# Optimization experiments

Hardware: AMD Instinct MI355X
Metric: run time of the kernel (lower is better)

Reference implementation:

```python
import jax, jax.numpy as jnp
from jax import lax
import numpy as np

FEAT_STRIDE = 16
N_PRE_NMS = 6000
N_POST_NMS = 300
NMS_THRESH = 0.7
MIN_SIZE = 16.0
HH, WW = 100, 152  # feature map size
IN_C, MID_C, N_ANCHOR = 512, 512, 9


def _anchor_base(base=16.0, ratios=(0.5, 1.0, 2.0), scales=(8, 16, 32)):
    py, px = base / 2.0, base / 2.0
    ab = np.zeros((len(ratios) * len(scales), 4), np.float32)
    for i, r in enumerate(ratios):
        for j, s in enumerate(scales):
            h = base * s * np.sqrt(r)
            w = base * s * np.sqrt(1.0 / r)
            ab[i * len(scales) + j] = [py - h / 2, px - w / 2, py + h / 2, px + w / 2]
    return ab


def _shifted_anchors(hh, ww, stride=FEAT_STRIDE):
    ab = _anchor_base()
    sy = np.arange(hh, dtype=np.float32) * stride
    sx = np.arange(ww, dtype=np.float32) * stride
    sx, sy = np.meshgrid(sx, sy)
    shift = np.stack((sy.ravel(), sx.ravel(), sy.ravel(), sx.ravel()), axis=1)
    # [K,A,4] -> [K*A,4]: location-major, anchor-minor (matches loc reshape order)
    return (shift[:, None, :] + ab[None, :, :]).reshape(-1, 4).astype(np.float32)


def _conv2d(x, w, b, pad):
    y = lax.conv_general_dilated(x, w, (1, 1), [(pad, pad), (pad, pad)],
                                 dimension_numbers=("NCHW", "OIHW", "NCHW"))
    return y + b[None, :, None, None]


def _loc2bbox(anchor, loc):
    h = anchor[:, 2] - anchor[:, 0]
    w = anchor[:, 3] - anchor[:, 1]
    cy = anchor[:, 0] + 0.5 * h
    cx = anchor[:, 1] + 0.5 * w
    dy, dx, dh, dw = loc[:, 0], loc[:, 1], loc[:, 2], loc[:, 3]
    cy2 = dy * h + cy
    cx2 = dx * w + cx
    h2 = jnp.exp(dh) * h
    w2 = jnp.exp(dw) * w
    return jnp.stack([cy2 - 0.5 * h2, cx2 - 0.5 * w2, cy2 + 0.5 * h2, cx2 + 0.5 * w2], axis=1)


def _nms_keep(boxes, thresh):
    # boxes sorted by score desc; sequential greedy NMS via fori_loop over a
    # precomputed [N,N] IoU matrix.
    N = boxes.shape[0]
    y1, x1, y2, x2 = boxes[:, 0], boxes[:, 1], boxes[:, 2], boxes[:, 3]
    area = (y2 - y1) * (x2 - x1)
    ih = jnp.clip(jnp.minimum(y2[:, None], y2[None, :]) - jnp.maximum(y1[:, None], y1[None, :]), 0.0)
    iw = jnp.clip(jnp.minimum(x2[:, None], x2[None, :]) - jnp.maximum(x1[:, None], x1[None, :]), 0.0)
    inter = ih * iw
    iou = inter / (area[:, None] + area[None, :] - inter + 1e-9)
    idx = jnp.arange(N)

    def body(i, keep):
        sup = keep[i] & (iou[i] > thresh) & (idx > i)
        return keep & ~sup

    return lax.fori_loop(0, N, body, jnp.ones((N,), bool))


def setup_inputs() -> dict:
    key = jax.random.key(0)
    ks = jax.random.split(key, 4)
    return {
        "x": jax.random.normal(ks[0], (1, IN_C, HH, WW), jnp.float32),
        "conv1_w": 0.01 * jax.random.normal(ks[1], (MID_C, IN_C, 3, 3), jnp.float32),
        "conv1_b": jnp.zeros((MID_C,), jnp.float32),
        "score_w": 0.01 * jax.random.normal(ks[2], (N_ANCHOR * 2, MID_C, 1, 1), jnp.float32),
        "score_b": jnp.zeros((N_ANCHOR * 2,), jnp.float32),
        "loc_w": 0.01 * jax.random.normal(ks[3], (N_ANCHOR * 4, MID_C, 1, 1), jnp.float32),
        "loc_b": jnp.zeros((N_ANCHOR * 4,), jnp.float32),
        "img_h": 1600,
        "img_w": 2432,
    }


def reference(x, conv1_w, conv1_b, score_w, score_b, loc_w, loc_b, img_h, img_w):
    n, _, hh, ww = x.shape
    anchors = jnp.asarray(_shifted_anchors(hh, ww))  # [hh*ww*A, 4]

    h = jax.nn.relu(_conv2d(x, conv1_w, conv1_b, 1))
    rpn_loc = _conv2d(h, loc_w, loc_b, 0).transpose(0, 2, 3, 1).reshape(n, -1, 4)
    scores_hw = _conv2d(h, score_w, score_b, 0).transpose(0, 2, 3, 1)  # [n,hh,ww,2A]
    fg = jax.nn.softmax(scores_hw.reshape(n, hh, ww, N_ANCHOR, 2), axis=-1)[..., 1].reshape(n, -1)
    rpn_score = scores_hw.reshape(n, -1, 2)

    # ProposalCreator (single image)
    roi = _loc2bbox(anchors, rpn_loc[0])
    roi = jnp.stack([
        jnp.clip(roi[:, 0], 0.0, img_h), jnp.clip(roi[:, 1], 0.0, img_w),
        jnp.clip(roi[:, 2], 0.0, img_h), jnp.clip(roi[:, 3], 0.0, img_w)], axis=1)
    valid = ((roi[:, 2] - roi[:, 0]) >= MIN_SIZE) & ((roi[:, 3] - roi[:, 1]) >= MIN_SIZE)
    sc = jnp.where(valid, fg[0], -jnp.inf)

    top_sc, order = lax.top_k(sc, N_PRE_NMS)
    roi_s = roi[order]  # sorted by score desc
    keep = _nms_keep(lax.stop_gradient(roi_s), NMS_THRESH) & (top_sc > -jnp.inf)
    sel_sc, sel = lax.top_k(jnp.where(keep, top_sc, -jnp.inf), N_POST_NMS)
    rois = jnp.where((sel_sc > -jnp.inf)[:, None], roi_s[sel], 0.0)  # [N_POST_NMS,4], zero-padded
    return rpn_loc, rpn_score, rois
```

## Files before the change

kernel.cpp:

```cpp
#include <hip/hip_runtime.h>
#include <math.h>
#include <stdint.h>

#define CHH 100
#define CWW 152
#define NPIX 15200
#define NANCH 136800
#define NPRE 6000
#define NPOST 300
#define CANDCAP 8192
#define MROW 96

#define PSTRIDE 154
#define PPVALID 16016
#define PPS 16128
#define XGUARD 256
#define XROWS_TOTAL (PPS + 2*XGUARD)

#define LPAD 32

#define WTH_OFF  0ull
#define WTL_OFF  4718592ull
#define WX_OFF   9437184ull
#define XH_OFF   9547776ull
#define XL_OFF   26587136ull
#define H_OFF    43626496ull
#define ROI_OFF  76656640ull
#define SC_OFF   78845440ull
#define CTL_OFF  79392640ull
#define CAND_OFF 79396736ull
#define SBOX_OFF 79462272ull

typedef _Float16 f16x8 __attribute__((ext_vector_type(8)));
typedef float    f32x4 __attribute__((ext_vector_type(4)));

struct Ctl {
  unsigned hist[256];
  unsigned prefix;
  unsigned countGreater;
  unsigned candCount;
  unsigned done;
};

struct AnchorArg { float v[36]; };

__device__ __forceinline__ unsigned mono_key(float f) {
  unsigned u = __float_as_uint(f);
  return u ^ ((u & 0x80000000u) ? 0xFFFFFFFFu : 0x80000000u);
}

__device__ __forceinline__ void async_copy16(void* lds, const void* g) {
  __builtin_amdgcn_global_load_lds(
      (const __attribute__((address_space(1))) unsigned int*)g,
      (__attribute__((address_space(3))) unsigned int*)lds,
      16, 0, 0);
}

__global__ __launch_bounds__(256) void prep_w_kernel(const float* __restrict__ w1,
                                                     _Float16* __restrict__ wtapH,
                                                     _Float16* __restrict__ wtapL,
                                                     const float* __restrict__ score_w,
                                                     const float* __restrict__ loc_w,
                                                     float* __restrict__ wx,
                                                     Ctl* __restrict__ ctl) {
  __shared__ float wl[4608];
  const int oc = blockIdx.x, tid = threadIdx.x;
  if (oc == 0) {
    ctl->hist[tid] = 0u;
    if (tid == 0) { ctl->prefix = 0u; ctl->countGreater = 0u; ctl->candCount = 0u; ctl->done = 0u; }
  }
  if (tid < 54) wx[oc * 54 + tid] = (tid < 18) ? score_w[tid * 512 + oc] : loc_w[(tid - 18) * 512 + oc];
  for (int li = tid; li < 4608; li += 256) wl[li] = w1[(size_t)oc * 4608 + li];
  __syncthreads();
  for (int t = 0; t < 9; ++t) {
    size_t ob = ((size_t)t * 512 + oc) * 512;
    for (int ic = tid; ic < 512; ic += 256) {
      float v = wl[ic * 9 + t];
      _Float16 hi = (_Float16)v;
      wtapH[ob + ic] = hi;
      wtapL[ob + ic] = (_Float16)(v - (float)hi);
    }
  }
}

__global__ __launch_bounds__(256) void prep_x_kernel(const float* __restrict__ x,
                                                     _Float16* __restrict__ xh,
                                                     _Float16* __restrict__ xl) {
  __shared__ float tile[64][65];
  const int tid = threadIdx.x;
  const int r0 = blockIdx.x * 64;
  for (int ic0 = 0; ic0 < 512; ic0 += 64) {
    #pragma unroll
    for (int it = 0; it < 16; ++it) {
      int li = it * 256 + tid;
      int i = li >> 6, j = li & 63;
      int pp = r0 + j - XGUARD;
      float v = 0.f;
      if (pp >= 0 && pp < PPVALID) {
        int rowp = pp / PSTRIDE, colp = pp - rowp * PSTRIDE;
        if (rowp >= 1 && rowp <= 100 && colp >= 1 && colp <= 152) {
          int p = (rowp - 1) * CWW + (colp - 1);
          v = x[(size_t)(ic0 + i) * NPIX + p];
        }
      }
      tile[i][j] = v;
    }
    __syncthreads();
    int j = tid >> 2, cq = tid & 3;
    size_t ob = (size_t)(r0 + j) * 512 + ic0 + cq * 16;
    f16x8 vh0, vh1, vl0, vl1;
    #pragma unroll
    for (int c = 0; c < 8; ++c) {
      float v = tile[cq * 16 + c][j];
      _Float16 hi = (_Float16)v;
      vh0[c] = hi; vl0[c] = (_Float16)(v - (float)hi);
    }
    #pragma unroll
    for (int c = 0; c < 8; ++c) {
      float v = tile[cq * 16 + 8 + c][j];
      _Float16 hi = (_Float16)v;
      vh1[c] = hi; vl1[c] = (_Float16)(v - (float)hi);
    }
    *(f16x8*)&xh[ob]     = vh0;
    *(f16x8*)&xh[ob + 8] = vh1;
    *(f16x8*)&xl[ob]     = vl0;
    *(f16x8*)&xl[ob + 8] = vl1;
    __syncthreads();
  }
}

__global__ __launch_bounds__(256) void conv1_mfma_kernel(const _Float16* __restrict__ xh,
                                                         const _Float16* __restrict__ xl,
                                                         const _Float16* __restrict__ wtapH,
                                                         const _Float16* __restrict__ wtapL,
                                                         const float* __restrict__ bias,
                                                         float* __restrict__ h) {
  __shared__ _Float16 Ah[2][128][LPAD], Al[2][128][LPAD], Bh[2][128][LPAD], Bl[2][128][LPAD];
  __shared__ float bsm[128];
  const int tid = threadIdx.x;
  const int bid = blockIdx.x;
  const int oc0 = (bid & 3) * 128;
  const int pp0 = (((bid >> 3) << 1) + ((bid >> 2) & 1)) * 128;
  if (tid < 128) bsm[tid] = bias[oc0 + tid];

  const int lane = tid & 63;
  const int n16 = lane & 15, quad = lane >> 4;
  const int wid = tid >> 6;
  const int wm = wid >> 1, wn = wid & 1;
  const int srow = tid >> 2, sq = tid & 3;
  const int wrow = wid << 4;
  const int sqs  = sq ^ ((srow >> 1) & 3);
  const int cswz = (n16 >> 1) & 3;
  const int rdc  = (quad ^ cswz) * 8;

  const size_t thBase = (size_t)srow * 512 + (size_t)sqs * 8;

  f32x4 acc[4][4];
  #pragma unroll
  for (int mi = 0; mi < 4; ++mi)
    #pragma unroll
    for (int ni = 0; ni < 4; ++ni) acc[mi][ni] = (f32x4){0.f, 0.f, 0.f, 0.f};

  auto stageF = [&](int b, int t, int icb, int dsh) {
    const size_t wOff = ((size_t)t * 512 + oc0) * 512 + (size_t)icb;
    const size_t xOff = (size_t)(pp0 + dsh) * 512 + (size_t)icb;
    #pragma unroll
    for (int hf = 0; hf < 2; ++hf) {
      const int lrow = hf * 64 + wrow;
      const size_t tho = thBase + (size_t)(hf * 64) * 512;
      async_copy16(&Ah[b][lrow][0], wtapH + wOff + tho);
      async_copy16(&Al[b][lrow][0], wtapL + wOff + tho);
      async_copy16(&Bh[b][lrow][0], xh + xOff + tho);
      async_copy16(&Bl[b][lrow][0], xl + xOff + tho);
    }
  };

  stageF(0, 0, 0, -PSTRIDE - 1);
  int tS = 1, icbS = 0, dshS = -PSTRIDE;

  asm volatile("s_waitcnt vmcnt(0)" ::: "memory");
  __builtin_amdgcn_sched_barrier(0);
  __builtin_amdgcn_s_barrier();
  __builtin_amdgcn_sched_barrier(0);

  for (int ks = 0; ks < 144; ++ks) {
    const int cur = ks & 1;
    if (ks + 1 < 144) {
      stageF(cur ^ 1, tS, icbS, dshS);
      if (++tS == 9) { tS = 0; icbS += 32; dshS = -PSTRIDE - 1; }
      else dshS += (tS == 3 || tS == 6) ? (PSTRIDE - 2) : 1;
    }

    __builtin_amdgcn_s_setprio(1);
    f16x8 af[4], ag[4], bf[4], bg[4];
    #pragma unroll
    for (int mi = 0; mi < 4; ++mi) {
      af[mi] = *(const f16x8*)&Ah[cur][wm * 64 + mi * 16 + n16][rdc];
      ag[mi] = *(const f16x8*)&Al[cur][wm * 64 + mi * 16 + n16][rdc];
    }
    #pragma unroll
    for (int ni = 0; ni < 4; ++ni) {
      bf[ni] = *(const f16x8*)&Bh[cur][wn * 64 + ni * 16 + n16][rdc];
      bg[ni] = *(const f16x8*)&Bl[cur][wn * 64 + ni * 16 + n16][rdc];
    }
    #pragma unroll
    for (int mi = 0; mi < 4; ++mi)
      #pragma unroll
      for (int ni = 0; ni < 4; ++ni) {
        acc[mi][ni] = __builtin_amdgcn_mfma_f32_16x16x32_f16(af[mi], bf[ni], acc[mi][ni], 0, 0, 0);
        acc[mi][ni] = __builtin_amdgcn_mfma_f32_16x16x32_f16(af[mi], bg[ni], acc[mi][ni], 0, 0, 0);
        acc[mi][ni] = __builtin_amdgcn_mfma_f32_16x16x32_f16(ag[mi], bf[ni], acc[mi][ni], 0, 0, 0);
      }
    __builtin_amdgcn_s_setprio(0);

    asm volatile("s_waitcnt lgkmcnt(0) vmcnt(0)" ::: "memory");
    __builtin_amdgcn_sched_barrier(0);
    __builtin_amdgcn_s_barrier();
    __builtin_amdgcn_sched_barrier(0);
  }

  #pragma unroll
  for (int mi = 0; mi < 4; ++mi) {
    int ocb = wm * 64 + mi * 16 + quad * 4;
    #pragma unroll
    for (int ni = 0; ni < 4; ++ni) {
      int pp = pp0 + wn * 64 + ni * 16 + n16;
      #pragma unroll
      for (int r = 0; r < 4; ++r) {
        float v = acc[mi][ni][r] + bsm[ocb + r];
        h[(size_t)(oc0 + ocb + r) * PPS + pp] = fmaxf(v, 0.f);
      }
    }
  }
}

__global__ __launch_bounds__(256) void heads_kernel(const float* __restrict__ h,
                                                    const float* __restrict__ wx,
                                                    const float* __restrict__ score_b,
                                                    const float* __restrict__ loc_b,
                                                    float* __restrict__ rpn_loc,
                                                    float* __restrict__ rpn_score,
                                                    float* __restrict__ roi,
                                                    float* __restrict__ sc,
                                                    AnchorArg ab,
                                                    const int* __restrict__ ihp,
                                                    const int* __restrict__ iwp) {
  __shared__ float hs[64][64];
  __shared__ float red[54][64];
  const int tid = threadIdx.x;
  const int p0 = blockIdx.x * 64;
  const int pxl = tid & 63, icq = tid >> 6;
  int pcol = p0 + pxl;
  bool pok = pcol < NPIX;
  int ppl = 0;
  if (pok) ppl = (pcol / CWW + 1) * PSTRIDE + (pcol % CWW) + 1;

  float acc[54];
  #pragma unroll
  for (int o = 0; o < 54; ++o) acc[o] = 0.f;

  for (int c = 0; c < 8; ++c) {
    int ic0 = c * 64;
    #pragma unroll
    for (int r = 0; r < 16; ++r) {
      int i = r * 4 + icq;
      hs[i][pxl] = pok ? h[(size_t)(ic0 + i) * PPS + ppl] : 0.f;
    }
    __syncthreads();
    #pragma unroll
    for (int k = 0; k < 16; ++k) {
      int icl = icq + k * 4;
      float v = hs[icl][pxl];
      const float* wrow = &wx[(ic0 + icl) * 54];
      #pragma unroll
      for (int o = 0; o < 54; ++o) acc[o] += wrow[o] * v;
    }
    __syncthreads();
  }
  for (int w = 0; w < 4; ++w) {
    if (icq == w) {
      if (w == 0) {
        #pragma unroll
        for (int o = 0; o < 54; ++o) red[o][pxl] = acc[o];
      } else {
        #pragma unroll
        for (int o = 0; o < 54; ++o) red[o][pxl] += acc[o];
      }
    }
    __syncthreads();
  }

  const float fH = (float)(*ihp);
  const float fW = (float)(*iwp);
  for (int it = tid; it < 576; it += 256) {
    #pragma clang fp contract(off)
    int pl = it / 9, a = it - pl * 9;
    int p = p0 + pl;
    if (p >= NPIX) continue;
    float s0 = red[a * 2][pl]     + score_b[a * 2];
    float s1 = red[a * 2 + 1][pl] + score_b[a * 2 + 1];
    float dy = red[18 + a * 4][pl]     + loc_b[a * 4];
    float dx = red[18 + a * 4 + 1][pl] + loc_b[a * 4 + 1];
    float dh = red[18 + a * 4 + 2][pl] + loc_b[a * 4 + 2];
    float dw = red[18 + a * 4 + 3][pl] + loc_b[a * 4 + 3];
    int row = p * 9 + a;
    *(float2*)&rpn_score[row * 2] = make_float2(s0, s1);
    *(float4*)&rpn_loc[(size_t)row * 4] = make_float4(dy, dx, dh, dw);
    int ypix = p / CWW, xpix = p - ypix * CWW;
    float sy = (float)(ypix * 16), sx = (float)(xpix * 16);
    float a0 = sy + ab.v[a * 4 + 0], a1 = sx + ab.v[a * 4 + 1];
    float a2 = sy + ab.v[a * 4 + 2], a3 = sx + ab.v[a * 4 + 3];
    float ha = a2 - a0, wa = a3 - a1;
    float cy = a0 + 0.5f * ha, cx = a1 + 0.5f * wa;
    float cy2 = dy * ha + cy, cx2 = dx * wa + cx;
    float h2 = expf(dh) * ha, w2 = expf(dw) * wa;
    float y1 = cy2 - 0.5f * h2, x1 = cx2 - 0.5f * w2;
    float y2 = cy2 + 0.5f * h2, x2 = cx2 + 0.5f * w2;
    y1 = fminf(fmaxf(y1, 0.f), fH); x1 = fminf(fmaxf(x1, 0.f), fW);
    y2 = fminf(fmaxf(y2, 0.f), fH); x2 = fminf(fmaxf(x2, 0.f), fW);
    *(float4*)&roi[(size_t)row * 4] = make_float4(y1, x1, y2, x2);
    bool valid = (y2 - y1 >= 16.f) && (x2 - x1 >= 16.f);
    float m  = fmaxf(s0, s1);
    float e0 = expf(s0 - m), e1 = expf(s1 - m);
    float fg = e1 / (e0 + e1);
    sc[row] = valid ? fg : -__builtin_inff();
  }
}

#define HGRID 120
__global__ __launch_bounds__(256) void hist_scan_kernel(const float* __restrict__ sc,
                                                        Ctl* __restrict__ ctl, int pass) {
  __shared__ unsigned hloc[256];
  __shared__ unsigned ticket_s;
  int tid = threadIdx.x;
  hloc[tid] = 0u;
  __syncthreads();
  unsigned prefix = ctl->prefix;
  for (int i = blockIdx.x * 256 + tid; i < NANCH; i += HGRID * 256) {
    unsigned m = mono_key(sc[i]);
    bool pred = (pass == 0) || ((m >> (32 - 8 * pass)) == prefix);
    if (pred) atomicAdd(&hloc[(m >> (24 - 8 * pass)) & 255u], 1u);
  }
  __syncthreads();
  if (hloc[tid]) atomicAdd(&ctl->hist[tid], hloc[tid]);
  __threadfence();
  __syncthreads();
  if (tid == 0) ticket_s = atomicAdd(&ctl->done, 1u);
  __syncthreads();
  if (ticket_s != HGRID - 1) return;
  unsigned v = atomicExch(&ctl->hist[tid], 0u);
  hloc[tid] = v;
  __syncthreads();
  for (int d = 1; d < 256; d <<= 1) {
    unsigned t2 = hloc[tid] + ((tid + d < 256) ? hloc[tid + d] : 0u);
    __syncthreads();
    hloc[tid] = t2;
    __syncthreads();
  }
  unsigned G = ctl->countGreater;
  unsigned inclT = hloc[tid];
  unsigned inclN = (tid < 255) ? hloc[tid + 1] : 0u;
  if (G + inclT >= (unsigned)NPRE && G + inclN < (unsigned)NPRE) {
    ctl->prefix = (prefix << 8) | (unsigned)tid;
    ctl->countGreater = G + inclN;
  }
  if (tid == 0) atomicExch(&ctl->done, 0u);
}

__global__ __launch_bounds__(256) void compact_kernel(const float* __restrict__ sc,
                                                      Ctl* __restrict__ ctl,
                                                      unsigned long long* __restrict__ cand) {
  int i = blockIdx.x * 256 + threadIdx.x;
  unsigned prefix = ctl->prefix;
  bool pred = false; unsigned m = 0;
  if (i < NANCH) { m = mono_key(sc[i]); pred = ((m >> 8) >= prefix); }
  unsigned long long mask = __ballot(pred);
  if (mask) {
    int lane = threadIdx.x & 63;
    int leader = __ffsll((long long)mask) - 1;
    unsigned base = 0;
    if (lane == leader) base = atomicAdd(&ctl->candCount, (unsigned)__popcll(mask));
    base = __shfl(base, leader);
    if (pred) {
      unsigned slot = base + (unsigned)__popcll(mask & ((1ull << lane) - 1ull));
      if (slot < CANDCAP)
        cand[slot] = (((unsigned long long)(~m)) << 32) | (unsigned)i;
    }
  }
}

__global__ __launch_bounds__(256) void rank_kernel(const unsigned long long* __restrict__ cand,
                                                   const Ctl* __restrict__ ctl,
                                                   const float* __restrict__ roi,
                                                   float4* __restrict__ sbox) {
  __shared__ unsigned long long kb[2048];
  __shared__ unsigned pc[64][5];
  const int tid = threadIdx.x;
  const int c = tid & 63, q = tid >> 6;
  const int slot = blockIdx.x * 64 + c;
  unsigned nv = ctl->candCount; if (nv > CANDCAP) nv = CANDCAP;
  unsigned long long K = (slot < (int)nv) ? cand[slot] : ~0ull;
  unsigned cnt = 0;
  for (unsigned c0 = 0; c0 < nv; c0 += 2048) {
    for (int i = tid; i < 2048; i += 256) {
      unsigned g = c0 + (unsigned)i;
      kb[i] = (g < nv) ? cand[g] : ~0ull;
    }
    __syncthreads();
    int lim = (int)(nv - c0); if (lim > 2048) lim = 2048;
    int i0 = q * 512, ie = i0 + 512; if (ie > lim) ie = lim;
    for (int i = i0; i < ie; ++i) cnt += (kb[i] < K) ? 1u : 0u;
    __syncthreads();
  }
  pc[c][q] = cnt;
  __syncthreads();
  if (q == 0) {
    unsigned rank = pc[c][0] + pc[c][1] + pc[c][2] + pc[c][3];
    if (slot < (int)nv && rank < NPRE) {
      unsigned idx = (unsigned)(K & 0xFFFFFFFFull);
      sbox[rank] = *(const float4*)&roi[(size_t)idx * 4];
    }
  } else if (q == 1) {
    int nvR = (nv < (unsigned)NPRE) ? (int)nv : NPRE;
    if (slot >= nvR && slot < NPRE) sbox[slot] = make_float4(0.f, 0.f, 0.f, 0.f);
  }
}

__device__ __forceinline__ bool iou_gt(float4 A, float4 B) {
  float areaA = (A.z - A.x) * (A.w - A.y);
  float areaB = (B.z - B.x) * (B.w - B.y);
  float ih = fmaxf(fminf(A.z, B.z) - fmaxf(A.x, B.x), 0.f);
  float iw = fmaxf(fminf(A.w, B.w) - fmaxf(A.y, B.y), 0.f);
  float inter = ih * iw;
  return inter / (areaA + areaB - inter + 1e-9f) > 0.7f;
}

__global__ __launch_bounds__(64) void mask_kernel(const float4* __restrict__ sbox,
                                                  unsigned long long* __restrict__ M) {
  const int ci = blockIdx.x, cj = blockIdx.y;
  if (cj < ci) return;
  __shared__ float4 cb[64];
  const int tid = threadIdx.x;
  const int i = ci * 64 + tid;
  const int jbase = cj * 64;
  const float4 bi = (i < NPRE) ? sbox[i] : make_float4(0.f, 0.f, 0.f, 0.f);
  cb[tid] = (jbase + tid < NPRE) ? sbox[jbase + tid] : make_float4(0.f, 0.f, 0.f, 0.f);
  __syncthreads();
  if (i >= NPRE) return;
  unsigned long long bits = 0ull;
  #pragma unroll 8
  for (int jj = 0; jj < 64; ++jj) {
    int jg = jbase + jj;
    float4 bj = cb[jj];
    if (jg > i && jg < NPRE && iou_gt(bi, bj)) bits |= (1ull << jj);
  }
  M[(size_t)i * MROW + cj] = bits;
}

__global__ __launch_bounds__(64) void resolve_kernel(const unsigned long long* __restrict__ M,
                                                     const Ctl* __restrict__ ctl,
                                                     const float4* __restrict__ sbox,
                                                     float* __restrict__ rois_out) {
  __shared__ unsigned long long remLDS[94];
  __shared__ int keepList[NPOST];
  __shared__ int keepCount;
  const int l = threadIdx.x;
  unsigned cnt = ctl->candCount; if (cnt > (unsigned)NPRE) cnt = NPRE;
  const int nvalid = (int)cnt;

  auto initw = [&](int w) -> unsigned long long {
    int lo = w * 64;
    if (lo + 64 <= nvalid) return 0ull;
    if (lo >= nvalid) return ~0ull;
    return (~0ull) << (nvalid - lo);
  };
  unsigned long long rem0 = initw(l);
  unsigned long long rem1 = (l < 30) ? initw(64 + l) : ~0ull;

  int keepTotal = 0;
  int cstop = 94;
  unsigned long long dw = M[(size_t)l * MROW + 0];

  for (int c = 0; c < 94; ++c) {
    unsigned long long dwN = 0ull;
    if (c + 1 < 94) dwN = M[(size_t)((c + 1) * 64 + l) * MROW + (c + 1)];

    unsigned long long remRep = (c < 64) ? __shfl(rem0, c) : __shfl(rem1, c - 64);

    #pragma unroll
    for (int kk = 0; kk < 64; kk += 16) {
      unsigned long long wv[16];
      #pragma unroll
      for (int t = 0; t < 16; ++t) wv[t] = __shfl(dw, kk + t);
      #pragma unroll
      for (int t = 0; t < 16; ++t) {
        if (!((remRep >> (kk + t)) & 1ull)) remRep |= wv[t];
      }
    }

    if (l == 0) remLDS[c] = remRep;
    if (c < 64) { if (l == c) rem0 = remRep; }
    else        { if (l == c - 64) rem1 = remRep; }
    keepTotal += (int)__popcll(~remRep);

    unsigned long long km = ~remRep;
    const size_t base = (size_t)c * 64;
    while (km) {
      int k0 = __ffsll((long long)km) - 1; km &= km - 1;
      int k1 = k0, k2 = k0, k3 = k0;
      if (km) { k1 = __ffsll((long long)km) - 1; km &= km - 1; }
      if (km) { k2 = __ffsll((long long)km) - 1; km &= km - 1; }
      if (km) { k3 = __ffsll((long long)km) - 1; km &= km - 1; }
      const unsigned long long* p0 = M + (base + k0) * MROW;
      const unsigned long long* p1 = M + (base + k1) * MROW;
      const unsigned long long* p2 = M + (base + k2) * MROW;
      const unsigned long long* p3 = M + (base + k3) * MROW;
      unsigned long long a0 = p0[l], a1 = p1[l], a2 = p2[l], a3 = p3[l];
      rem0 |= a0 | a1 | a2 | a3;
      if (l < 30) {
        unsigned long long b0 = p0[64 + l], b1 = p1[64 + l], b2 = p2[64 + l], b3 = p3[64 + l];
        rem1 |= b0 | b1 | b2 | b3;
      }
    }

    dw = dwN;
    if (keepTotal >= NPOST) { cstop = c + 1; break; }
  }

  __syncthreads();
  if (l == 0) {
    int ck = 0;
    for (int w = 0; w < cstop && ck < NPOST; ++w) {
      unsigned long long kw = ~remLDS[w];
      while (kw && ck < NPOST) {
        int r = __ffsll((long long)kw) - 1; kw &= kw - 1;
        keepList[ck++] = w * 64 + r;
      }
    }
    keepCount = ck;
  }
  __syncthreads();
  for (int s = l; s < NPOST; s += 64) {
    float4 b = make_float4(0.f, 0.f, 0.f, 0.f);
    if (s < keepCount) b = sbox[keepList[s]];
    *(float4*)&rois_out[(size_t)s * 4] = b;
  }
}

extern "C" void kernel_launch(void* const* d_in, const int* in_sizes, int n_in,
                              void* d_out, int out_size, void* d_ws, size_t ws_size,
                              hipStream_t stream) {
  const float* x  = (const float*)d_in[0];
  const float* w1 = (const float*)d_in[1];
  const float* b1 = (const float*)d_in[2];
  const float* sw = (const float*)d_in[3];
  const float* sb = (const float*)d_in[4];
  const float* lw = (const float*)d_in[5];
  const float* lb = (const float*)d_in[6];
  const int* ihp  = (const int*)d_in[7];
  const int* iwp  = (const int*)d_in[8];
  float* out = (float*)d_out;

  char* ws = (char*)d_ws;
  _Float16* wtapH = (_Float16*)(ws + WTH_OFF);
  _Float16* wtapL = (_Float16*)(ws + WTL_OFF);
  float* wx   = (float*)(ws + WX_OFF);
  _Float16* xh_alloc = (_Float16*)(ws + XH_OFF);
  _Float16* xl_alloc = (_Float16*)(ws + XL_OFF);
  _Float16* xh = xh_alloc + (size_t)XGUARD * 512;
  _Float16* xl = xl_alloc + (size_t)XGUARD * 512;
  float* h    = (float*)(ws + H_OFF);
  float* roi  = (float*)(ws + ROI_OFF);
  float* sc   = (float*)(ws + SC_OFF);
  Ctl*   ctl  = (Ctl*)(ws + CTL_OFF);
  unsigned long long* cand = (unsigned long long*)(ws + CAND_OFF);
  float4* sbox = (float4*)(ws + SBOX_OFF);
  unsigned long long* Mmask = (unsigned long long*)(ws + H_OFF);

  AnchorArg ab;
  {
    const double ratios[3] = {0.5, 1.0, 2.0};
    const double scales[3] = {8.0, 16.0, 32.0};
    for (int i = 0; i < 3; ++i)
      for (int j = 0; j < 3; ++j) {
        double hh = 16.0 * scales[j] * sqrt(ratios[i]);
        double wwd = 16.0 * scales[j] * sqrt(1.0 / ratios[i]);
        int a = i * 3 + j;
        ab.v[a * 4 + 0] = (float)(8.0 - hh / 2.0);
        ab.v[a * 4 + 1] = (float)(8.0 - wwd / 2.0);
        ab.v[a * 4 + 2] = (float)(8.0 + hh / 2.0);
        ab.v[a * 4 + 3] = (float)(8.0 + wwd / 2.0);
      }
  }

  float* rpn_loc   = out;
  float* rpn_score = out + 547200;
  float* rois      = out + 820800;

  prep_w_kernel<<<512, 256, 0, stream>>>(w1, wtapH, wtapL, sw, lw, wx, ctl);
  prep_x_kernel<<<XROWS_TOTAL / 64, 256, 0, stream>>>(x, xh_alloc, xl_alloc);
  conv1_mfma_kernel<<<504, 256, 0, stream>>>(xh, xl, wtapH, wtapL, b1, h);
  heads_kernel<<<238, 256, 0, stream>>>(h, wx, sb, lb, rpn_loc, rpn_score, roi, sc, ab, ihp, iwp);
  for (int p = 0; p < 3; ++p)
    hist_scan_kernel<<<HGRID, 256, 0, stream>>>(sc, ctl, p);
  compact_kernel<<<535, 256, 0, stream>>>(sc, ctl, cand);
  rank_kernel<<<CANDCAP / 64, 256, 0, stream>>>(cand, ctl, roi, sbox);
  mask_kernel<<<dim3(94, 94), 64, 0, stream>>>(sbox, Mmask);
  resolve_kernel<<<1, 64, 0, stream>>>(Mmask, ctl, sbox, rois);
}
```

Baseline: 648.9 us.

## Enlarge conv1 tiles to 256x256 with split-K halves and atomic accumulation

```diff
diff --git a/kernel.cpp b/kernel.cpp
--- a/kernel.cpp
+++ b/kernel.cpp
@@ -129,24 +129,22 @@
   }
 }
 
-__global__ __launch_bounds__(256) void conv1_mfma_kernel(const _Float16* __restrict__ xh,
+__global__ __launch_bounds__(512) void conv1_mfma_kernel(const _Float16* __restrict__ xh,
                                                          const _Float16* __restrict__ xl,
                                                          const _Float16* __restrict__ wtapH,
                                                          const _Float16* __restrict__ wtapL,
-                                                         const float* __restrict__ bias,
                                                          float* __restrict__ h) {
-  __shared__ _Float16 Ah[2][128][LPAD], Al[2][128][LPAD], Bh[2][128][LPAD], Bl[2][128][LPAD];
-  __shared__ float bsm[128];
+  __shared__ _Float16 Ah[2][256][LPAD], Al[2][256][LPAD], Bh[2][256][LPAD], Bl[2][256][LPAD];
   const int tid = threadIdx.x;
   const int bid = blockIdx.x;
-  const int oc0 = (bid & 3) * 128;
-  const int pp0 = (((bid >> 3) << 1) + ((bid >> 2) & 1)) * 128;
-  if (tid < 128) bsm[tid] = bias[oc0 + tid];
+  const int oc0 = (bid & 1) * 256;
+  const int KH  = (bid >> 1) & 1;
+  const int pp0 = (bid >> 2) * 256;
 
   const int lane = tid & 63;
   const int n16 = lane & 15, quad = lane >> 4;
   const int wid = tid >> 6;
-  const int wm = wid >> 1, wn = wid & 1;
+  const int wm = wid >> 2, wn = wid & 3;
   const int srow = tid >> 2, sq = tid & 3;
   const int wrow = wid << 4;
   const int sqs  = sq ^ ((srow >> 1) & 3);
@@ -155,9 +153,9 @@
 
   const size_t thBase = (size_t)srow * 512 + (size_t)sqs * 8;
 
-  f32x4 acc[4][4];
+  f32x4 acc[8][4];
   #pragma unroll
-  for (int mi = 0; mi < 4; ++mi)
+  for (int mi = 0; mi < 8; ++mi)
     #pragma unroll
     for (int ni = 0; ni < 4; ++ni) acc[mi][ni] = (f32x4){0.f, 0.f, 0.f, 0.f};
 
@@ -166,8 +164,8 @@
     const size_t xOff = (size_t)(pp0 + dsh) * 512 + (size_t)icb;
     #pragma unroll
     for (int hf = 0; hf < 2; ++hf) {
-      const int lrow = hf * 64 + wrow;
-      const size_t tho = thBase + (size_t)(hf * 64) * 512;
+      const int lrow = hf * 128 + wrow;
+      const size_t tho = thBase + (size_t)(hf * 128) * 512;
       async_copy16(&Ah[b][lrow][0], wtapH + wOff + tho);
       async_copy16(&Al[b][lrow][0], wtapL + wOff + tho);
       async_copy16(&Bh[b][lrow][0], xh + xOff + tho);
@@ -175,42 +173,42 @@
     }
   };
 
-  stageF(0, 0, 0, -PSTRIDE - 1);
-  int tS = 1, icbS = 0, dshS = -PSTRIDE;
+  const int icBase = KH * 256;
+  stageF(0, 0, icBase, -PSTRIDE - 1);
+  int tS = 1, icbS = icBase, dshS = -PSTRIDE;
 
   asm volatile("s_waitcnt vmcnt(0)" ::: "memory");
   __builtin_amdgcn_sched_barrier(0);
   __builtin_amdgcn_s_barrier();
   __builtin_amdgcn_sched_barrier(0);
 
-  for (int ks = 0; ks < 144; ++ks) {
+  for (int ks = 0; ks < 72; ++ks) {
     const int cur = ks & 1;
-    if (ks + 1 < 144) {
+    if (ks + 1 < 72) {
       stageF(cur ^ 1, tS, icbS, dshS);
       if (++tS == 9) { tS = 0; icbS += 32; dshS = -PSTRIDE - 1; }
       else dshS += (tS == 3 || tS == 6) ? (PSTRIDE - 2) : 1;
     }
 
     __builtin_amdgcn_s_setprio(1);
-    f16x8 af[4], ag[4], bf[4], bg[4];
-    #pragma unroll
-    for (int mi = 0; mi < 4; ++mi) {
-      af[mi] = *(const f16x8*)&Ah[cur][wm * 64 + mi * 16 + n16][rdc];
-      ag[mi] = *(const f16x8*)&Al[cur][wm * 64 + mi * 16 + n16][rdc];
-    }
+    f16x8 bf[4], bg[4];
     #pragma unroll
     for (int ni = 0; ni < 4; ++ni) {
       bf[ni] = *(const f16x8*)&Bh[cur][wn * 64 + ni * 16 + n16][rdc];
       bg[ni] = *(const f16x8*)&Bl[cur][wn * 64 + ni * 16 + n16][rdc];
     }
     #pragma unroll
-    for (int mi = 0; mi < 4; ++mi)
+    for (int mi = 0; mi < 8; ++mi) {
+      f16x8 af = *(const f16x8*)&Ah[cur][wm * 128 + mi * 16 + n16][rdc];
+      f16x8 ag = *(const f16x8*)&Al[cur][wm * 128 + mi * 16 + n16][rdc];
       #pragma unroll
       for (int ni = 0; ni < 4; ++ni) {
-        acc[mi][ni] = __builtin_amdgcn_mfma_f32_16x16x32_f16(af[mi], bf[ni], acc[mi][ni], 0, 0, 0);
-        acc[mi][ni] = __builtin_amdgcn_mfma_f32_16x16x32_f16(af[mi], bg[ni], acc[mi][ni], 0, 0, 0);
-        acc[mi][ni] = __builtin_amdgcn_mfma_f32_16x16x32_f16(ag[mi], bf[ni], acc[mi][ni], 0, 0, 0);
+        acc[mi][ni] = __builtin_amdgcn_mfma_f32_16x16x32_f16(af, bf[ni], acc[mi][ni], 0, 0, 0);
+        acc[mi][ni] = __builtin_amdgcn_mfma_f32_16x16x32_f16(af, bg[ni], acc[mi][ni], 0, 0, 0);
+        acc[mi][ni] = __builtin_amdgcn_mfma_f32_16x16x32_f16(ag, bf[ni], acc[mi][ni], 0, 0, 0);
       }
+      if (mi == 3) __builtin_amdgcn_sched_barrier(0);
+    }
     __builtin_amdgcn_s_setprio(0);
 
     asm volatile("s_waitcnt lgkmcnt(0) vmcnt(0)" ::: "memory");
@@ -220,21 +218,20 @@
   }
 
   #pragma unroll
-  for (int mi = 0; mi < 4; ++mi) {
-    int ocb = wm * 64 + mi * 16 + quad * 4;
+  for (int mi = 0; mi < 8; ++mi) {
+    int ocb = oc0 + wm * 128 + mi * 16 + quad * 4;
     #pragma unroll
     for (int ni = 0; ni < 4; ++ni) {
       int pp = pp0 + wn * 64 + ni * 16 + n16;
       #pragma unroll
-      for (int r = 0; r < 4; ++r) {
-        float v = acc[mi][ni][r] + bsm[ocb + r];
-        h[(size_t)(oc0 + ocb + r) * PPS + pp] = fmaxf(v, 0.f);
-      }
+      for (int r = 0; r < 4; ++r)
+        atomicAdd(&h[(size_t)(ocb + r) * PPS + pp], acc[mi][ni][r]);
     }
   }
 }
 
 __global__ __launch_bounds__(256) void heads_kernel(const float* __restrict__ h,
+                                                    const float* __restrict__ conv_b,
                                                     const float* __restrict__ wx,
                                                     const float* __restrict__ score_b,
                                                     const float* __restrict__ loc_b,
@@ -264,7 +261,7 @@
     #pragma unroll
     for (int r = 0; r < 16; ++r) {
       int i = r * 4 + icq;
-      hs[i][pxl] = pok ? h[(size_t)(ic0 + i) * PPS + ppl] : 0.f;
+      hs[i][pxl] = pok ? fmaxf(h[(size_t)(ic0 + i) * PPS + ppl] + conv_b[ic0 + i], 0.f) : 0.f;
     }
     __syncthreads();
     #pragma unroll
@@ -599,8 +596,9 @@
 
   prep_w_kernel<<<512, 256, 0, stream>>>(w1, wtapH, wtapL, sw, lw, wx, ctl);
   prep_x_kernel<<<XROWS_TOTAL / 64, 256, 0, stream>>>(x, xh_alloc, xl_alloc);
-  conv1_mfma_kernel<<<504, 256, 0, stream>>>(xh, xl, wtapH, wtapL, b1, h);
-  heads_kernel<<<238, 256, 0, stream>>>(h, wx, sb, lb, rpn_loc, rpn_score, roi, sc, ab, ihp, iwp);
+  hipMemsetAsync(h, 0, (size_t)512 * PPS * sizeof(float), stream);
+  conv1_mfma_kernel<<<252, 512, 0, stream>>>(xh, xl, wtapH, wtapL, h);
+  heads_kernel<<<238, 256, 0, stream>>>(h, b1, wx, sb, lb, rpn_loc, rpn_score, roi, sc, ab, ihp, iwp);
   for (int p = 0; p < 3; ++p)
     hist_scan_kernel<<<HGRID, 256, 0, stream>>>(sc, ctl, p);
   compact_kernel<<<535, 256, 0, stream>>>(sc, ctl, cand);
```

Result: slower. 679.2 us (+4.7%).
